# Kernel optimization log

Hardware: AMD Instinct MI355X
Metric: run time of the kernel (lower is better)

The kernel has to match this reference:

```python
import jax, jax.numpy as jnp
import numpy as np

DIM = 256          # channels
HEADS = 8
KS = 3             # kernel_size
DIL = (1, 2, 3, 4) # dilation rates
ND = len(DIL)
HEAD_DIM = DIM // HEADS
SCALE = HEAD_DIM ** -0.5
DPG = DIM // ND    # channels per dilation group
EPS = 1e-5


def setup_inputs() -> dict:
    key = jax.random.key(0)
    ks = jax.random.split(key, 4)
    B, H, W = 8, 64, 64
    vi = jax.random.normal(ks[0], (B, DIM, H, W), jnp.float32)
    ir = jax.random.normal(ks[1], (B, DIM, H, W), jnp.float32)
    w_qkv = jax.random.normal(ks[2], (3 * DIM, DIM), jnp.float32) * 0.02  # 1x1 conv, no bias (qkv_bias=False)
    proj_w = jax.random.normal(ks[3], (DIM, DIM), jnp.float32) * 0.02     # nn.Linear weight
    proj_b = jnp.zeros((DIM,), jnp.float32)
    ln_g = jnp.ones((DIM,), jnp.float32)
    ln_b = jnp.zeros((DIM,), jnp.float32)
    return dict(vi=vi, ir=ir, w_qkv=w_qkv, proj_w=proj_w, proj_b=proj_b, ln_g=ln_g, ln_b=ln_b)


def _unfold(t, dil):
    # t: [B, d, H, W] -> [B, d, KS*KS, H, W], same layout as nn.Unfold(KS, dil, pad=dil*(KS-1)//2)
    B, d, H, W = t.shape
    pad = dil * (KS - 1) // 2
    tp = jnp.pad(t, ((0, 0), (0, 0), (pad, pad), (pad, pad)))
    patches = [tp[:, :, i * dil:i * dil + H, j * dil:j * dil + W]
               for i in range(KS) for j in range(KS)]
    return jnp.stack(patches, axis=2)


def _dilate_attention(q, k, v, dil):
    # q,k,v: [B, d, H, W] with d = DPG; returns [B, H, W, d]
    B, d, H, W = q.shape
    h = d // HEAD_DIM
    N = H * W
    kk = KS * KS
    qf = q.reshape(B, h, HEAD_DIM, N)                      # b h d n
    kf = _unfold(k, dil).reshape(B, h, HEAD_DIM, kk, N)    # b h d k n
    vf = _unfold(v, dil).reshape(B, h, HEAD_DIM, kk, N)
    attn = jax.nn.softmax(jnp.einsum('bhdn,bhdkn->bhnk', qf, kf) * SCALE, axis=-1)
    out = jnp.einsum('bhnk,bhdkn->bhnd', attn, vf)         # b h n d
    return out.transpose(0, 2, 1, 3).reshape(B, H, W, d)   # channel = head*HEAD_DIM + c


def _dilate_block(x, w_qkv, proj_w, proj_b, ln_g, ln_b):
    # x: [B, C, H, W]; DilateBlock: permute -> LN -> MultiDilatelocalAttention -> residual -> permute back
    B, C, H, W = x.shape
    xn = x.transpose(0, 2, 3, 1)                           # B H W C
    mu = jnp.mean(xn, -1, keepdims=True)
    var = jnp.var(xn, -1, keepdims=True)
    xn = (xn - mu) * jax.lax.rsqrt(var + EPS) * ln_g + ln_b
    xc = xn.transpose(0, 3, 1, 2)                          # B C H W
    # 1x1 conv qkv -> [B, 3, ND, DPG, H, W]
    qkv = jnp.einsum('oc,bchw->bohw', w_qkv, xc).reshape(B, 3, ND, DPG, H, W)
    outs = [_dilate_attention(qkv[:, 0, i], qkv[:, 1, i], qkv[:, 2, i], DIL[i])
            for i in range(ND)]                            # each [B, H, W, DPG]
    y = jnp.stack(outs, axis=3).reshape(B, H, W, C)        # channel = dil_idx*DPG + c
    y = y @ proj_w.T + proj_b                              # nn.Linear
    return x + y.transpose(0, 3, 1, 2)                     # residual, back to B C H W


def reference(vi, ir, w_qkv, proj_w, proj_b, ln_g, ln_b):
    sub = vi - ir
    div = _dilate_block(sub, w_qkv, proj_w, proj_b, ln_g, ln_b)
    o = jnp.matmul(vi, div)   # batched [H,W]@[H,W] over (B, C)
    return (o, o)
```

## Files before the change

### kernel.cpp

```cpp
#include <hip/hip_runtime.h>
#include <math.h>

#define B_ 8
#define C_ 256
#define N_ 4096
#define NPOS 32768
#define SCALE_ 0.1767766952966369f
#define EPS_ 1e-5f

typedef __attribute__((ext_vector_type(8))) short bf16x8;
typedef __attribute__((ext_vector_type(8))) unsigned short u16x8;
typedef __attribute__((ext_vector_type(4))) float f32x4;

__device__ __forceinline__ unsigned short f2bf(float f) {
  union { float f; unsigned u; } v; v.f = f;
  unsigned r = v.u + 0x7fff + ((v.u >> 16) & 1);
  return (unsigned short)(r >> 16);
}
__device__ __forceinline__ float bf2f(unsigned short u) {
  union { unsigned u; float f; } v; v.u = ((unsigned)u) << 16; return v.f;
}
__device__ __forceinline__ float blo(unsigned u) {
  union { unsigned u; float f; } v; v.u = u << 16; return v.f;
}
__device__ __forceinline__ float bhi(unsigned u) {
  union { unsigned u; float f; } v; v.u = u & 0xffff0000u; return v.f;
}

#define GLD_LDS16(g, l) \
  __builtin_amdgcn_global_load_lds((const __attribute__((address_space(1))) unsigned int*)(g), \
                                   (__attribute__((address_space(3))) unsigned int*)(l), 16, 0, 0)

__global__ __launch_bounds__(256) void k_cvt(
    const float* __restrict__ wq, const float* __restrict__ pw,
    unsigned short* __restrict__ dst)
{
  int i4 = blockIdx.x * 256 + threadIdx.x;
  float4 v = (i4 < 49152) ? ((const float4*)wq)[i4] : ((const float4*)pw)[i4 - 49152];
  ushort4 o;
  o.x = f2bf(v.x); o.y = f2bf(v.y); o.z = f2bf(v.z); o.w = f2bf(v.w);
  ((ushort4*)dst)[i4] = o;
}

__global__ __launch_bounds__(256) void k_sub_ln(
    const float* __restrict__ vi, const float* __restrict__ ir,
    const float* __restrict__ ln_g, const float* __restrict__ ln_b,
    float* __restrict__ sub, unsigned short* __restrict__ xn)
{
  __shared__ float tile[C_ * 33];
  __shared__ float redS[8][32], redS2[8][32];
  __shared__ float meanS[32], rstdS[32];
  int blk = blockIdx.x;
  int b = blk >> 7;
  int y = (blk >> 1) & 63;
  int half = blk & 1;
  int t = threadIdx.x;
  size_t base = (size_t)b * C_ * N_ + (size_t)y * 64 + half * 32;
  #pragma unroll 4
  for (int it = 0; it < 32; ++it) {
    int c = it * 8 + (t >> 5);
    int x = t & 31;
    size_t g = base + (size_t)c * N_ + x;
    float s = vi[g] - ir[g];
    sub[g] = s;
    tile[c * 33 + x] = s;
  }
  __syncthreads();
  {
    int p = t & 31, grp = t >> 5;
    float s = 0.f, s2 = 0.f;
    #pragma unroll
    for (int cc = 0; cc < 32; ++cc) {
      float v = tile[(grp * 32 + cc) * 33 + p];
      s += v; s2 += v * v;
    }
    redS[grp][p] = s; redS2[grp][p] = s2;
  }
  __syncthreads();
  if (t < 32) {
    float s = 0.f, s2 = 0.f;
    #pragma unroll
    for (int g2 = 0; g2 < 8; ++g2) { s += redS[g2][t]; s2 += redS2[g2][t]; }
    float mu = s * (1.f / 256.f);
    float var = s2 * (1.f / 256.f) - mu * mu;
    meanS[t] = mu;
    rstdS[t] = rsqrtf(var + EPS_);
  }
  __syncthreads();
  int c = t;
  float gg = ln_g[c], bb = ln_b[c];
  size_t xbase = ((size_t)b * N_ + (size_t)y * 64 + half * 32) * C_;
  for (int p = 0; p < 32; ++p) {
    float v = (tile[c * 33 + p] - meanS[p]) * rstdS[p] * gg + bb;
    xn[xbase + (size_t)p * C_ + c] = f2bf(v);
  }
}

template<int EPI>
__global__ __launch_bounds__(256) void k_gemm_mfma(
    const unsigned short* __restrict__ A,
    const unsigned short* __restrict__ Bw,
    void* __restrict__ Cout,
    const float* __restrict__ bias,
    const float* __restrict__ sub,
    int ldc)
{
  __shared__ __align__(16) unsigned short As[128 * 32];
  __shared__ __align__(16) unsigned short Bs[128 * 32];
  int tid = threadIdx.x;
  int wv = tid >> 6;
  int lane = tid & 63;
  int m0 = blockIdx.x * 128;
  int n0 = blockIdx.y * 128;
  int mw = (wv >> 1) * 64, nw = (wv & 1) * 64;
  int r = lane & 15, q = lane >> 4;

  int seg0 = wv * 2;
  int srow0 = seg0 * 16 + (lane >> 2);
  int scol = (lane & 3) * 8;
  const unsigned short* ga0 = A  + (size_t)(m0 + srow0) * 256 + scol;
  const unsigned short* ga1 = ga0 + 16 * 256;
  const unsigned short* gb0 = Bw + (size_t)(n0 + srow0) * 256 + scol;
  const unsigned short* gb1 = gb0 + 16 * 256;
  unsigned short* la0 = &As[seg0 * 512];
  unsigned short* la1 = la0 + 512;
  unsigned short* lb0 = &Bs[seg0 * 512];
  unsigned short* lb1 = lb0 + 512;

  f32x4 acc[4][4];
  #pragma unroll
  for (int i = 0; i < 4; ++i)
    #pragma unroll
    for (int j = 0; j < 4; ++j)
      acc[i][j] = (f32x4){0.f, 0.f, 0.f, 0.f};

  for (int k0 = 0; k0 < 256; k0 += 32) {
    GLD_LDS16(ga0 + k0, la0);
    GLD_LDS16(ga1 + k0, la1);
    GLD_LDS16(gb0 + k0, lb0);
    GLD_LDS16(gb1 + k0, lb1);
    __syncthreads();
    bf16x8 af[4], bfr[4];
    #pragma unroll
    for (int mt = 0; mt < 4; ++mt)
      af[mt] = *(const bf16x8*)&As[(mw + mt * 16 + r) * 32 + q * 8];
    #pragma unroll
    for (int nt = 0; nt < 4; ++nt)
      bfr[nt] = *(const bf16x8*)&Bs[(nw + nt * 16 + r) * 32 + q * 8];
    #pragma unroll
    for (int mt = 0; mt < 4; ++mt)
      #pragma unroll
      for (int nt = 0; nt < 4; ++nt)
        acc[mt][nt] = __builtin_amdgcn_mfma_f32_16x16x32_bf16(af[mt], bfr[nt], acc[mt][nt], 0, 0, 0);
    __syncthreads();
  }

  if (EPI == 0) {
    unsigned short* C = (unsigned short*)Cout;
    #pragma unroll
    for (int mt = 0; mt < 4; ++mt)
      #pragma unroll
      for (int nt = 0; nt < 4; ++nt) {
        int n = n0 + nw + nt * 16 + r;
        #pragma unroll
        for (int rr = 0; rr < 4; ++rr) {
          int m = m0 + mw + mt * 16 + q * 4 + rr;
          C[(size_t)m * ldc + n] = f2bf(acc[mt][nt][rr]);
        }
      }
  } else {
    float* divm = (float*)Cout;
    #pragma unroll
    for (int mt = 0; mt < 4; ++mt) {
      int p0 = m0 + mw + mt * 16 + q * 4;
      int b = p0 >> 12, nn = p0 & 4095;
      #pragma unroll
      for (int nt = 0; nt < 4; ++nt) {
        int c = n0 + nw + nt * 16 + r;
        size_t idx = ((size_t)(b * 256 + c)) * 4096 + nn;
        float4 s4 = *(const float4*)&sub[idx];
        float bb = bias[c];
        float4 o;
        o.x = s4.x + bb + acc[mt][nt][0];
        o.y = s4.y + bb + acc[mt][nt][1];
        o.z = s4.z + bb + acc[mt][nt][2];
        o.w = s4.w + bb + acc[mt][nt][3];
        *(float4*)&divm[idx] = o;
      }
    }
  }
}

__global__ __launch_bounds__(256) void k_attn(
    const unsigned short* __restrict__ qkv,
    unsigned short* __restrict__ y)
{
  int t = threadIdx.x;
  int sub = t >> 2;
  int lane4 = t & 3;
  int item = blockIdx.x * 64 + sub;
  int ih = item & 7;
  int p = item >> 3;
  int i = ih >> 1, h = ih & 1;
  int dil = i + 1;
  int b = p >> 12;
  int n = p & 4095;
  int py = n >> 6, px = n & 63;
  int off = i * 64 + h * 32 + lane4 * 8;
  const unsigned short* base = qkv + off;

  uint4 qw = *(const uint4*)(base + (size_t)p * 768);
  float q0 = blo(qw.x), q1 = bhi(qw.x), q2 = blo(qw.y), q3 = bhi(qw.y),
        q4 = blo(qw.z), q5 = bhi(qw.z), q6 = blo(qw.w), q7 = bhi(qw.w);

  int pj[9];
  #pragma unroll
  for (int j = 0; j < 9; ++j) {
    int ny = py + (j / 3 - 1) * dil;
    int nx = px + (j % 3 - 1) * dil;
    bool ok = ((unsigned)ny < 64u) && ((unsigned)nx < 64u);
    pj[j] = ok ? ((b << 12) + (ny << 6) + nx) : -1;
  }

  float sc[9];
  #pragma unroll
  for (int j = 0; j < 9; ++j) {
    float s = 0.f;
    if (pj[j] >= 0) {
      uint4 kw = *(const uint4*)(base + 256 + (size_t)pj[j] * 768);
      s  = q0 * blo(kw.x) + q1 * bhi(kw.x);
      s += q2 * blo(kw.y) + q3 * bhi(kw.y);
      s += q4 * blo(kw.z) + q5 * bhi(kw.z);
      s += q6 * blo(kw.w) + q7 * bhi(kw.w);
    }
    s += __shfl_xor(s, 1, 4);
    s += __shfl_xor(s, 2, 4);
    sc[j] = s * SCALE_;
  }

  float mx = sc[0];
  #pragma unroll
  for (int j = 1; j < 9; ++j) mx = fmaxf(mx, sc[j]);
  float e[9], ssum = 0.f;
  #pragma unroll
  for (int j = 0; j < 9; ++j) { e[j] = __expf(sc[j] - mx); ssum += e[j]; }
  float inv = 1.f / ssum;

  float o0 = 0.f, o1 = 0.f, o2 = 0.f, o3 = 0.f, o4 = 0.f, o5 = 0.f, o6 = 0.f, o7 = 0.f;
  #pragma unroll
  for (int j = 0; j < 9; ++j) {
    if (pj[j] >= 0) {
      float w = e[j] * inv;
      uint4 vw = *(const uint4*)(base + 512 + (size_t)pj[j] * 768);
      o0 += w * blo(vw.x); o1 += w * bhi(vw.x);
      o2 += w * blo(vw.y); o3 += w * bhi(vw.y);
      o4 += w * blo(vw.z); o5 += w * bhi(vw.z);
      o6 += w * blo(vw.w); o7 += w * bhi(vw.w);
    }
  }

  u16x8 ov;
  ov[0] = f2bf(o0); ov[1] = f2bf(o1); ov[2] = f2bf(o2); ov[3] = f2bf(o3);
  ov[4] = f2bf(o4); ov[5] = f2bf(o5); ov[6] = f2bf(o6); ov[7] = f2bf(o7);
  *(u16x8*)(y + (size_t)p * 256 + off) = ov;
}

__global__ __launch_bounds__(256) void k_bmm(
    const float* __restrict__ vi, const float* __restrict__ divm,
    float* __restrict__ out)
{
  __shared__ float At[64 * 68];
  __shared__ float Bsm[64 * 64];
  int bc = blockIdx.x;
  size_t base = (size_t)bc * 4096;
  int t = threadIdx.x;
  #pragma unroll
  for (int it = 0; it < 4; ++it) {
    int flat = it * 1024 + t * 4;
    int row = flat >> 6, col = flat & 63;
    float4 a = *(const float4*)&vi[base + flat];
    float4 bv = *(const float4*)&divm[base + flat];
    At[(col + 0) * 68 + row] = a.x;
    At[(col + 1) * 68 + row] = a.y;
    At[(col + 2) * 68 + row] = a.z;
    At[(col + 3) * 68 + row] = a.w;
    *(float4*)&Bsm[flat] = bv;
  }
  __syncthreads();
  int tx = t & 15, ty = t >> 4;
  float acc[4][4] = {};
  for (int k = 0; k < 64; ++k) {
    float4 a = *(const float4*)&At[k * 68 + (ty << 2)];
    float4 b = *(const float4*)&Bsm[k * 64 + (tx << 2)];
    acc[0][0] += a.x * b.x; acc[0][1] += a.x * b.y; acc[0][2] += a.x * b.z; acc[0][3] += a.x * b.w;
    acc[1][0] += a.y * b.x; acc[1][1] += a.y * b.y; acc[1][2] += a.y * b.z; acc[1][3] += a.y * b.w;
    acc[2][0] += a.z * b.x; acc[2][1] += a.z * b.y; acc[2][2] += a.z * b.z; acc[2][3] += a.z * b.w;
    acc[3][0] += a.w * b.x; acc[3][1] += a.w * b.y; acc[3][2] += a.w * b.z; acc[3][3] += a.w * b.w;
  }
  #pragma unroll
  for (int i = 0; i < 4; ++i) {
    int row = (ty << 2) + i;
    float4 w = make_float4(acc[i][0], acc[i][1], acc[i][2], acc[i][3]);
    *(float4*)&out[base + row * 64 + (tx << 2)] = w;
    *(float4*)&out[8388608ull + base + row * 64 + (tx << 2)] = w;
  }
}

extern "C" void kernel_launch(void* const* d_in, const int* in_sizes, int n_in,
                              void* d_out, int out_size, void* d_ws, size_t ws_size,
                              hipStream_t stream) {
  const float* vi     = (const float*)d_in[0];
  const float* ir     = (const float*)d_in[1];
  const float* w_qkv  = (const float*)d_in[2];
  const float* proj_w = (const float*)d_in[3];
  const float* proj_b = (const float*)d_in[4];
  const float* ln_g   = (const float*)d_in[5];
  const float* ln_b   = (const float*)d_in[6];
  float* out = (float*)d_out;
  char* ws = (char*)d_ws;
  float*          sub  = (float*)(ws);
  unsigned short* qkvb = (unsigned short*)(ws + 33554432);
  float*          divm = (float*)(ws + 33554432);
  unsigned short* xnb  = (unsigned short*)(ws + 83886080);
  unsigned short* yb   = (unsigned short*)(ws + 100663296);
  unsigned short* wqb  = (unsigned short*)(ws + 117440512);
  unsigned short* pwb  = wqb + 196608;

  k_cvt<<<256, 256, 0, stream>>>(w_qkv, proj_w, wqb);
  k_sub_ln<<<1024, 256, 0, stream>>>(vi, ir, ln_g, ln_b, sub, xnb);
  k_gemm_mfma<0><<<dim3(256, 6), 256, 0, stream>>>(xnb, wqb, (void*)qkvb, nullptr, nullptr, 768);
  k_attn<<<4096, 256, 0, stream>>>(qkvb, yb);
  k_gemm_mfma<1><<<dim3(256, 2), 256, 0, stream>>>(yb, pwb, (void*)divm, proj_b, sub, 0);
  k_bmm<<<2048, 256, 0, stream>>>(vi, divm, out);
}
```

Before: 225.4 us.

## Store residual and div intermediates in bf16 and stage GEMM epilogues through LDS

The residual (vi-ir) and the block output div are now stored as bf16 instead of fp32, which halves their global write and read traffic across sub_ln, the proj GEMM epilogue and the batched matmul. The GEMM epilogues now stage results through an LDS tile so global stores become coalesced 16-byte vectors rather than scattered 2- or 4-byte writes. The sub_ln load loop is also vectorised to float4. The cost is extra rounding on the residual path and on div before the final fp32 matmul, which may hurt accuracy.

```diff
diff --git a/kernel.cpp b/kernel.cpp
--- a/kernel.cpp
+++ b/kernel.cpp
@@ -10,6 +10,7 @@
 
 typedef __attribute__((ext_vector_type(8))) short bf16x8;
 typedef __attribute__((ext_vector_type(8))) unsigned short u16x8;
+typedef __attribute__((ext_vector_type(4))) unsigned short u16x4;
 typedef __attribute__((ext_vector_type(4))) float f32x4;
 
 __device__ __forceinline__ unsigned short f2bf(float f) {
@@ -45,7 +46,7 @@
 __global__ __launch_bounds__(256) void k_sub_ln(
     const float* __restrict__ vi, const float* __restrict__ ir,
     const float* __restrict__ ln_g, const float* __restrict__ ln_b,
-    float* __restrict__ sub, unsigned short* __restrict__ xn)
+    unsigned short* __restrict__ subB, unsigned short* __restrict__ xn)
 {
   __shared__ float tile[C_ * 33];
   __shared__ float redS[8][32], redS2[8][32];
@@ -56,14 +57,22 @@
   int half = blk & 1;
   int t = threadIdx.x;
   size_t base = (size_t)b * C_ * N_ + (size_t)y * 64 + half * 32;
-  #pragma unroll 4
-  for (int it = 0; it < 32; ++it) {
-    int c = it * 8 + (t >> 5);
-    int x = t & 31;
-    size_t g = base + (size_t)c * N_ + x;
-    float s = vi[g] - ir[g];
-    sub[g] = s;
-    tile[c * 33 + x] = s;
+  #pragma unroll
+  for (int it = 0; it < 8; ++it) {
+    int c = it * 32 + (t >> 3);
+    int xq = (t & 7) * 4;
+    size_t g = base + (size_t)c * N_ + xq;
+    float4 v4 = *(const float4*)&vi[g];
+    float4 i4 = *(const float4*)&ir[g];
+    float4 s4;
+    s4.x = v4.x - i4.x; s4.y = v4.y - i4.y; s4.z = v4.z - i4.z; s4.w = v4.w - i4.w;
+    ushort4 sb;
+    sb.x = f2bf(s4.x); sb.y = f2bf(s4.y); sb.z = f2bf(s4.z); sb.w = f2bf(s4.w);
+    *(ushort4*)&subB[g] = sb;
+    tile[c * 33 + xq + 0] = s4.x;
+    tile[c * 33 + xq + 1] = s4.y;
+    tile[c * 33 + xq + 2] = s4.z;
+    tile[c * 33 + xq + 3] = s4.w;
   }
   __syncthreads();
   {
@@ -100,13 +109,14 @@
 __global__ __launch_bounds__(256) void k_gemm_mfma(
     const unsigned short* __restrict__ A,
     const unsigned short* __restrict__ Bw,
-    void* __restrict__ Cout,
+    unsigned short* __restrict__ Cout,
     const float* __restrict__ bias,
-    const float* __restrict__ sub,
+    const unsigned short* __restrict__ subB,
     int ldc)
 {
   __shared__ __align__(16) unsigned short As[128 * 32];
   __shared__ __align__(16) unsigned short Bs[128 * 32];
+  __shared__ __align__(16) unsigned short Cs[64 * 136];
   int tid = threadIdx.x;
   int wv = tid >> 6;
   int lane = tid & 63;
@@ -155,37 +165,65 @@
     __syncthreads();
   }
 
-  if (EPI == 0) {
-    unsigned short* C = (unsigned short*)Cout;
-    #pragma unroll
-    for (int mt = 0; mt < 4; ++mt)
-      #pragma unroll
-      for (int nt = 0; nt < 4; ++nt) {
-        int n = n0 + nw + nt * 16 + r;
+  int b = m0 >> 12;
+  int nn0 = m0 & 4095;
+  #pragma unroll
+  for (int pass = 0; pass < 2; ++pass) {
+    __syncthreads();
+    if (EPI == 0) {
+      if ((wv >> 1) == pass) {
         #pragma unroll
-        for (int rr = 0; rr < 4; ++rr) {
-          int m = m0 + mw + mt * 16 + q * 4 + rr;
-          C[(size_t)m * ldc + n] = f2bf(acc[mt][nt][rr]);
+        for (int mt = 0; mt < 4; ++mt) {
+          int lr = mt * 16 + q * 4;
+          #pragma unroll
+          for (int nt = 0; nt < 4; ++nt) {
+            int col = nw + nt * 16 + r;
+            #pragma unroll
+            for (int rr = 0; rr < 4; ++rr)
+              Cs[(lr + rr) * 136 + col] = f2bf(acc[mt][nt][rr]);
+          }
         }
       }
-  } else {
-    float* divm = (float*)Cout;
-    #pragma unroll
-    for (int mt = 0; mt < 4; ++mt) {
-      int p0 = m0 + mw + mt * 16 + q * 4;
-      int b = p0 >> 12, nn = p0 & 4095;
+    } else {
+      if ((wv & 1) == pass) {
+        #pragma unroll
+        for (int nt = 0; nt < 4; ++nt) {
+          int lr = nt * 16 + r;
+          #pragma unroll
+          for (int mt = 0; mt < 4; ++mt) {
+            int pc = mw + mt * 16 + q * 4;
+            #pragma unroll
+            for (int rr = 0; rr < 4; ++rr)
+              Cs[lr * 136 + pc + rr] = f2bf(acc[mt][nt][rr]);
+          }
+        }
+      }
+    }
+    __syncthreads();
+    if (EPI == 0) {
       #pragma unroll
-      for (int nt = 0; nt < 4; ++nt) {
-        int c = n0 + nw + nt * 16 + r;
-        size_t idx = ((size_t)(b * 256 + c)) * 4096 + nn;
-        float4 s4 = *(const float4*)&sub[idx];
+      for (int cc = 0; cc < 4; ++cc) {
+        int ch = cc * 256 + tid;
+        int row = ch >> 4, cg = ch & 15;
+        u16x8 cv = *(const u16x8*)&Cs[row * 136 + cg * 8];
+        int m = m0 + pass * 64 + row;
+        *(u16x8*)&Cout[(size_t)m * ldc + n0 + cg * 8] = cv;
+      }
+    } else {
+      #pragma unroll
+      for (int cc = 0; cc < 4; ++cc) {
+        int ch = cc * 256 + tid;
+        int row = ch >> 4, cg = ch & 15;
+        u16x8 cv = *(const u16x8*)&Cs[row * 136 + cg * 8];
+        int c = n0 + pass * 64 + row;
+        size_t idx = ((size_t)(b * 256 + c)) * 4096 + nn0 + cg * 8;
+        u16x8 sv = *(const u16x8*)&subB[idx];
         float bb = bias[c];
-        float4 o;
-        o.x = s4.x + bb + acc[mt][nt][0];
-        o.y = s4.y + bb + acc[mt][nt][1];
-        o.z = s4.z + bb + acc[mt][nt][2];
-        o.w = s4.w + bb + acc[mt][nt][3];
-        *(float4*)&divm[idx] = o;
+        u16x8 ov;
+        #pragma unroll
+        for (int e = 0; e < 8; ++e)
+          ov[e] = f2bf(bf2f((unsigned short)cv[e]) + bb + bf2f((unsigned short)sv[e]));
+        *(u16x8*)&Cout[idx] = ov;
       }
     }
   }
@@ -266,7 +304,7 @@
 }
 
 __global__ __launch_bounds__(256) void k_bmm(
-    const float* __restrict__ vi, const float* __restrict__ divm,
+    const float* __restrict__ vi, const unsigned short* __restrict__ divmB,
     float* __restrict__ out)
 {
   __shared__ float At[64 * 68];
@@ -279,12 +317,22 @@
     int flat = it * 1024 + t * 4;
     int row = flat >> 6, col = flat & 63;
     float4 a = *(const float4*)&vi[base + flat];
-    float4 bv = *(const float4*)&divm[base + flat];
     At[(col + 0) * 68 + row] = a.x;
     At[(col + 1) * 68 + row] = a.y;
     At[(col + 2) * 68 + row] = a.z;
     At[(col + 3) * 68 + row] = a.w;
-    *(float4*)&Bsm[flat] = bv;
+  }
+  #pragma unroll
+  for (int it = 0; it < 2; ++it) {
+    int flat = it * 2048 + t * 8;
+    u16x8 dv = *(const u16x8*)&divmB[base + flat];
+    float4 lo, hi;
+    lo.x = bf2f((unsigned short)dv[0]); lo.y = bf2f((unsigned short)dv[1]);
+    lo.z = bf2f((unsigned short)dv[2]); lo.w = bf2f((unsigned short)dv[3]);
+    hi.x = bf2f((unsigned short)dv[4]); hi.y = bf2f((unsigned short)dv[5]);
+    hi.z = bf2f((unsigned short)dv[6]); hi.w = bf2f((unsigned short)dv[7]);
+    *(float4*)&Bsm[flat] = lo;
+    *(float4*)&Bsm[flat + 4] = hi;
   }
   __syncthreads();
   int tx = t & 15, ty = t >> 4;
@@ -318,18 +366,18 @@
   const float* ln_b   = (const float*)d_in[6];
   float* out = (float*)d_out;
   char* ws = (char*)d_ws;
-  float*          sub  = (float*)(ws);
-  unsigned short* qkvb = (unsigned short*)(ws + 33554432);
-  float*          divm = (float*)(ws + 33554432);
-  unsigned short* xnb  = (unsigned short*)(ws + 83886080);
-  unsigned short* yb   = (unsigned short*)(ws + 100663296);
-  unsigned short* wqb  = (unsigned short*)(ws + 117440512);
+  unsigned short* subB = (unsigned short*)(ws);
+  unsigned short* qkvb = (unsigned short*)(ws + 16777216);
+  unsigned short* divmB= (unsigned short*)(ws + 16777216);
+  unsigned short* xnb  = (unsigned short*)(ws + 67108864);
+  unsigned short* yb   = (unsigned short*)(ws + 83886080);
+  unsigned short* wqb  = (unsigned short*)(ws + 100663296);
   unsigned short* pwb  = wqb + 196608;
 
   k_cvt<<<256, 256, 0, stream>>>(w_qkv, proj_w, wqb);
-  k_sub_ln<<<1024, 256, 0, stream>>>(vi, ir, ln_g, ln_b, sub, xnb);
-  k_gemm_mfma<0><<<dim3(256, 6), 256, 0, stream>>>(xnb, wqb, (void*)qkvb, nullptr, nullptr, 768);
+  k_sub_ln<<<1024, 256, 0, stream>>>(vi, ir, ln_g, ln_b, subB, xnb);
+  k_gemm_mfma<0><<<dim3(256, 6), 256, 0, stream>>>(xnb, wqb, qkvb, nullptr, nullptr, 768);
   k_attn<<<4096, 256, 0, stream>>>(qkvb, yb);
-  k_gemm_mfma<1><<<dim3(256, 2), 256, 0, stream>>>(yb, pwb, (void*)divm, proj_b, sub, 0);
-  k_bmm<<<2048, 256, 0, stream>>>(vi, divm, out);
-}
+  k_gemm_mfma<1><<<dim3(256, 2), 256, 0, stream>>>(yb, pwb, divmB, proj_b, subB, 0);
+  k_bmm<<<2048, 256, 0, stream>>>(vi, divmB, out);
+}
```

Result: faster. 215.4 us (-4.4%).
